# Kernel optimization log

Measured on AMD Instinct MI355X. Metric: run time of the kernel, lower is better.

Reference implementation:

```python
import jax, jax.numpy as jnp
import numpy as np

NEG_INF = -9e15  # matches torch's -9000000000000000.0 mask value
LEAKY_SLOPE = 0.2  # init alpha


def setup_inputs() -> dict:
    key = jax.random.key(0)
    k1, k2, k3, k4 = jax.random.split(key, 4)
    N, dim = 4096, 128
    hidden = jax.random.normal(k1, (N, dim), dtype=jnp.float32)
    adj = jax.random.randint(k2, (N, N), 0, 5)  # relation codes 0..4
    W = jax.random.normal(k3, (4, dim), dtype=jnp.float32) * (1.0 / np.sqrt(dim))
    b = jax.random.normal(k4, (4,), dtype=jnp.float32) * 0.01
    return {"hidden": hidden, "adj": adj, "W": W, "b": b}


def reference(hidden, adj, W, b):
    # e_k[i,j] = leakyrelu(sum_d h[i,d]*h[j,d]*W[k,d] + b[k])
    # equivalent to the torch repeat/view outer-product + four dim->1 Linears,
    # computed without materializing the [N,N,dim] intermediate.
    hw = hidden[None, :, :] * W[:, None, :]               # [4, N, dim]
    e = jnp.einsum('knd,md->knm', hw, hidden) + b[:, None, None]  # [4, N, N]
    e = jax.nn.leaky_relu(e, negative_slope=LEAKY_SLOPE)
    neg = jnp.asarray(NEG_INF, dtype=e.dtype)
    alpha = jnp.where(adj == 1, e[0], neg)
    alpha = jnp.where(adj == 2, e[1], alpha)
    alpha = jnp.where(adj == 3, e[2], alpha)
    alpha = jnp.where(adj == 4, e[3], alpha)
    alpha = jax.nn.softmax(alpha, axis=-1)                # [N, N]
    return alpha @ hidden                                  # [N, dim]
```

## Files before the change

kernel.cpp:

```cpp
#include <hip/hip_runtime.h>

#define NN 4096
#define DIM 128
#define TN 64
#define TM 128
#define NSPLIT 4
#define NTILES 8

typedef __attribute__((ext_vector_type(8))) short bf16x8;
typedef __attribute__((ext_vector_type(4))) float f32x4;

#define LSTRIDE 136
#define REGION  (128 * LSTRIDE)
#define TILE_USH (2 * REGION)
#define TILE_CHUNKS 68
#define PST 136

__device__ inline unsigned short f2bf(float x) {
    union { float f; unsigned u; } v; v.f = x;
    unsigned r = v.u + 0x7FFFu + ((v.u >> 16) & 1u);
    return (unsigned short)(r >> 16);
}

__device__ inline void dma16(const void* g, void* l) {
    __builtin_amdgcn_global_load_lds(
        (const __attribute__((address_space(1))) void*)g,
        (__attribute__((address_space(3))) void*)l,
        16, 0, 0);
}

__global__ __launch_bounds__(256) void prep_pack_kernel(
    const float* __restrict__ hidden,
    unsigned short* __restrict__ Hpack)
{
    __shared__ unsigned short T[16][LSTRIDE];
    const int tid = threadIdx.x;
    const int t0  = blockIdx.x >> 3;
    const int s   = blockIdx.x & 7;
    const int m0  = t0 * TM;
    unsigned short* rowdst = Hpack + (size_t)t0 * TILE_USH;
    unsigned short* coldst = rowdst + REGION;

    #pragma unroll
    for (int it = 0; it < 2; ++it) {
        int idx = tid + 256 * it;
        int row = idx >> 5;
        int c4  = (idx & 31) * 4;
        float4 v = *(const float4*)(hidden + (size_t)(m0 + 16 * s + row) * DIM + c4);
        ushort4 o;
        o.x = f2bf(v.x); o.y = f2bf(v.y); o.z = f2bf(v.z); o.w = f2bf(v.w);
        *(ushort4*)(rowdst + (16 * s + row) * LSTRIDE + c4) = o;
    }
    #pragma unroll
    for (int it = 0; it < 2; ++it) {
        int idx = tid + 256 * it;
        int m  = idx >> 2;
        int dc = (idx & 3) * 4;
        float4 v = *(const float4*)(hidden + (size_t)(m0 + m) * DIM + 16 * s + dc);
        T[dc + 0][m] = f2bf(v.x);
        T[dc + 1][m] = f2bf(v.y);
        T[dc + 2][m] = f2bf(v.z);
        T[dc + 3][m] = f2bf(v.w);
    }
    __syncthreads();
    {
        int d  = tid >> 4;
        int c8 = (tid & 15) * 8;
        uint4 v = *(const uint4*)(&T[d][c8]);
        *(uint4*)(coldst + (16 * s + d) * LSTRIDE + c8) = v;
    }
}

__global__ __launch_bounds__(512, 2) void gat_flash_kernel(
    const float* __restrict__ hidden,
    const unsigned short* __restrict__ Hpack,
    const int*   __restrict__ adj,
    const float* __restrict__ W,
    const float* __restrict__ bvec,
    float*       __restrict__ Opart,
    float*       __restrict__ lpart)
{
    __shared__ __align__(16) unsigned short HH[2][TILE_USH];
    __shared__ __align__(16) unsigned short Plc[TN * PST];
    __shared__ float redsum[8][16];

    const int tid  = threadIdx.x;
    const int w    = tid >> 6;
    const int lane = tid & 63;
    const int g    = lane >> 4;
    const int l15  = lane & 15;
    const int blk  = blockIdx.x;
    const int nbr  = blk >> 2;
    const int q4   = blk & 3;
    const int n0   = nbr * TN;
    const int gt0  = q4 * NTILES;
    const int rg   = w >> 1;
    const int msw  = w & 1;
    const int lofs = lane * 16;
    const float NEG = -9.0e15f;

    const float b0 = bvec[0], b1 = bvec[1], b2 = bvec[2], b3 = bvec[3];

    {
        const char* src = (const char*)(Hpack + (size_t)gt0 * TILE_USH);
        char* dst = (char*)&HH[0][0];
        #pragma unroll
        for (int it = 0; it < 9; ++it) {
            int chunk = it * 8 + w;
            if (chunk < TILE_CHUNKS)
                dma16(src + chunk * 1024 + lofs, dst + chunk * 1024);
        }
    }
    {
        #pragma unroll
        for (int it = 0; it < 4; ++it) {
            int idx = tid + 512 * it;
            int row = idx >> 3;
            int c16 = (idx & 7) * 16;
            int k = row >> 6, r = row & 63;
            const float* hrow = hidden + (size_t)(n0 + r) * DIM + c16;
            const float* wrow = W + k * DIM + c16;
            unsigned short* qdst = &HH[1][row * LSTRIDE + c16];
            #pragma unroll
            for (int c = 0; c < 4; ++c) {
                float4 hv = *(const float4*)(hrow + 4 * c);
                float4 wv = *(const float4*)(wrow + 4 * c);
                ushort4 o;
                o.x = f2bf(hv.x * wv.x); o.y = f2bf(hv.y * wv.y);
                o.z = f2bf(hv.z * wv.z); o.w = f2bf(hv.w * wv.w);
                *(ushort4*)(qdst + 4 * c) = o;
            }
        }
    }
    __syncthreads();

    bf16x8 Af[4][4];
    #pragma unroll
    for (int k = 0; k < 4; ++k)
        #pragma unroll
        for (int ks = 0; ks < 4; ++ks)
            Af[k][ks] = *(const bf16x8*)&HH[1][(k * 64 + rg * 16 + l15) * LSTRIDE + ks * 32 + 8 * g];
    __syncthreads();

    float lrow[4] = {0.f, 0.f, 0.f, 0.f};
    f32x4 Oacc[4];
    #pragma unroll
    for (int dt = 0; dt < 4; ++dt) Oacc[dt] = (f32x4){0.f, 0.f, 0.f, 0.f};

    const size_t arow = (size_t)(n0 + rg * 16 + 4 * g) * NN;
    int avc[16], avn[16];
    #pragma unroll
    for (int ch = 0; ch < 4; ++ch)
        #pragma unroll
        for (int t = 0; t < 4; ++t)
            avc[ch * 4 + t] = adj[arow + (size_t)t * NN + gt0 * TM + msw * 64 + ch * 16 + l15];

    for (int tile = 0; tile < NTILES; ++tile) {
        const int cur = tile & 1;
        const int nxt = cur ^ 1;

        if (tile + 1 < NTILES) {
            const char* src = (const char*)(Hpack + (size_t)(gt0 + tile + 1) * TILE_USH);
            char* dst = (char*)&HH[nxt][0];
            #pragma unroll
            for (int it = 0; it < 9; ++it) {
                int chunk = it * 8 + w;
                if (chunk < TILE_CHUNKS)
                    dma16(src + chunk * 1024 + lofs, dst + chunk * 1024);
            }
            #pragma unroll
            for (int ch = 0; ch < 4; ++ch)
                #pragma unroll
                for (int t = 0; t < 4; ++t)
                    avn[ch * 4 + t] = adj[arow + (size_t)t * NN + (gt0 + tile + 1) * TM + msw * 64 + ch * 16 + l15];
        }

        f32x4 S[4][4];
        #pragma unroll
        for (int k = 0; k < 4; ++k)
            #pragma unroll
            for (int ch = 0; ch < 4; ++ch)
                S[k][ch] = (f32x4){0.f, 0.f, 0.f, 0.f};
        #pragma unroll
        for (int ks = 0; ks < 4; ++ks) {
            #pragma unroll
            for (int ch = 0; ch < 4; ++ch) {
                bf16x8 B = *(const bf16x8*)&HH[cur][(msw * 64 + ch * 16 + l15) * LSTRIDE + ks * 32 + 8 * g];
                #pragma unroll
                for (int k = 0; k < 4; ++k)
                    S[k][ch] = __builtin_amdgcn_mfma_f32_16x16x32_bf16(Af[k][ks], B, S[k][ch], 0, 0, 0);
            }
        }

        #pragma unroll
        for (int ch = 0; ch < 4; ++ch) {
            #pragma unroll
            for (int t = 0; t < 4; ++t) {
                int a = avc[ch * 4 + t];
                float s = S[0][ch][t] + b0;
                s = (a == 2) ? S[1][ch][t] + b1 : s;
                s = (a == 3) ? S[2][ch][t] + b2 : s;
                s = (a == 4) ? S[3][ch][t] + b3 : s;
                float e = fmaxf(s, 0.2f * s);
                e = (a == 0) ? NEG : e;
                float p = __expf(e);
                lrow[t] += p;
                Plc[(rg * 16 + 4 * g + t) * PST + msw * 64 + ch * 16 + l15] = f2bf(p);
            }
        }

        asm volatile("s_waitcnt lgkmcnt(0)\n\ts_barrier" ::: "memory");

        #pragma unroll
        for (int c4 = 0; c4 < 4; ++c4) {
            bf16x8 Pa = *(const bf16x8*)&Plc[(rg * 16 + l15) * PST + c4 * 32 + 8 * g];
            #pragma unroll
            for (int dt = 0; dt < 4; ++dt) {
                bf16x8 Bv = *(const bf16x8*)&HH[cur][REGION + (msw * 64 + dt * 16 + l15) * LSTRIDE + c4 * 32 + 8 * g];
                Oacc[dt] = __builtin_amdgcn_mfma_f32_16x16x32_bf16(Pa, Bv, Oacc[dt], 0, 0, 0);
            }
        }

        #pragma unroll
        for (int i = 0; i < 16; ++i) avc[i] = avn[i];
        __syncthreads();
    }

    #pragma unroll
    for (int t = 0; t < 4; ++t) {
        float v = lrow[t];
        v += __shfl_xor(v, 1); v += __shfl_xor(v, 2);
        v += __shfl_xor(v, 4); v += __shfl_xor(v, 8);
        if (l15 == 0) redsum[w][4 * g + t] = v;
    }
    __syncthreads();
    if (tid < TN) {
        int rg2 = tid >> 4, rr = tid & 15;
        lpart[blk * TN + tid] = redsum[rg2 * 2 + 0][rr] + redsum[rg2 * 2 + 1][rr];
    }
    float* Ob = Opart + (size_t)blk * (TN * DIM);
    #pragma unroll
    for (int dt = 0; dt < 4; ++dt)
        #pragma unroll
        for (int t = 0; t < 4; ++t)
            Ob[(rg * 16 + 4 * g + t) * DIM + msw * 64 + dt * 16 + l15] = Oacc[dt][t];
}

__global__ __launch_bounds__(256) void combine_kernel(
    const float* __restrict__ Opart, const float* __restrict__ lpart,
    float* __restrict__ out)
{
    int idx = blockIdx.x * 256 + threadIdx.x;
    int r = idx >> 7, d = idx & 127;
    int nbr = r >> 6, rr = r & 63;
    float O = 0.f, l = 0.f;
    #pragma unroll
    for (int q = 0; q < NSPLIT; ++q) {
        O += Opart[(size_t)(nbr * NSPLIT + q) * (TN * DIM) + rr * 128 + d];
        l += lpart[(nbr * NSPLIT + q) * TN + rr];
    }
    out[idx] = O / l;
}

extern "C" void kernel_launch(void* const* d_in, const int* in_sizes, int n_in,
                              void* d_out, int out_size, void* d_ws, size_t ws_size,
                              hipStream_t stream) {
    const float* hidden = (const float*)d_in[0];
    const int*   adj    = (const int*)d_in[1];
    const float* W      = (const float*)d_in[2];
    const float* b      = (const float*)d_in[3];
    float* out = (float*)d_out;

    char* ws = (char*)d_ws;
    unsigned short* Hpack = (unsigned short*)ws;
    float* Opart = (float*)(ws + (4u << 20));
    float* lpart = (float*)(ws + (12u << 20));

    prep_pack_kernel<<<(NN / TM) * 8, 256, 0, stream>>>(hidden, Hpack);
    gat_flash_kernel<<<256, 512, 0, stream>>>(hidden, Hpack, adj, W, b, Opart, lpart);
    combine_kernel<<<NN * DIM / 256, 256, 0, stream>>>(Opart, lpart, out);
}
```

Baseline: 131.5 us.

## Double threads per block to 1024 and split tile columns across four warps

The flash-style GAT kernel now launches 1024 threads per block, so 16 waves each own 32 columns of a tile instead of 64. Per-wave score and output accumulators shrink, and the score MFMAs are interleaved per column chunk to cut register pressure. The aim is more latency hiding within each block, since there are only 256 blocks. The masked case now zeroes the probability after exp rather than feeding a huge negative into exp. The trade-off is that each wave reloads the same A fragments for less work, and the larger block may not fit two blocks per CU.

```diff
diff --git a/kernel.cpp b/kernel.cpp
--- a/kernel.cpp
+++ b/kernel.cpp
@@ -71,7 +71,7 @@
     }
 }
 
-__global__ __launch_bounds__(512, 2) void gat_flash_kernel(
+__global__ __launch_bounds__(1024) void gat_flash_kernel(
     const float* __restrict__ hidden,
     const unsigned short* __restrict__ Hpack,
     const int*   __restrict__ adj,
@@ -82,7 +82,7 @@
 {
     __shared__ __align__(16) unsigned short HH[2][TILE_USH];
     __shared__ __align__(16) unsigned short Plc[TN * PST];
-    __shared__ float redsum[8][16];
+    __shared__ float redsum[16][16];
 
     const int tid  = threadIdx.x;
     const int w    = tid >> 6;
@@ -94,10 +94,9 @@
     const int q4   = blk & 3;
     const int n0   = nbr * TN;
     const int gt0  = q4 * NTILES;
-    const int rg   = w >> 1;
-    const int msw  = w & 1;
+    const int rg   = w >> 2;
+    const int msw  = w & 3;
     const int lofs = lane * 16;
-    const float NEG = -9.0e15f;
 
     const float b0 = bvec[0], b1 = bvec[1], b2 = bvec[2], b3 = bvec[3];
 
@@ -105,16 +104,16 @@
         const char* src = (const char*)(Hpack + (size_t)gt0 * TILE_USH);
         char* dst = (char*)&HH[0][0];
         #pragma unroll
-        for (int it = 0; it < 9; ++it) {
-            int chunk = it * 8 + w;
+        for (int it = 0; it < 5; ++it) {
+            int chunk = it * 16 + w;
             if (chunk < TILE_CHUNKS)
                 dma16(src + chunk * 1024 + lofs, dst + chunk * 1024);
         }
     }
     {
         #pragma unroll
-        for (int it = 0; it < 4; ++it) {
-            int idx = tid + 512 * it;
+        for (int it = 0; it < 2; ++it) {
+            int idx = tid + 1024 * it;
             int row = idx >> 3;
             int c16 = (idx & 7) * 16;
             int k = row >> 6, r = row & 63;
@@ -143,17 +142,17 @@
     __syncthreads();
 
     float lrow[4] = {0.f, 0.f, 0.f, 0.f};
-    f32x4 Oacc[4];
-    #pragma unroll
-    for (int dt = 0; dt < 4; ++dt) Oacc[dt] = (f32x4){0.f, 0.f, 0.f, 0.f};
+    f32x4 Oacc[2];
+    #pragma unroll
+    for (int dt = 0; dt < 2; ++dt) Oacc[dt] = (f32x4){0.f, 0.f, 0.f, 0.f};
 
     const size_t arow = (size_t)(n0 + rg * 16 + 4 * g) * NN;
-    int avc[16], avn[16];
-    #pragma unroll
-    for (int ch = 0; ch < 4; ++ch)
+    int avc[8], avn[8];
+    #pragma unroll
+    for (int ch = 0; ch < 2; ++ch)
         #pragma unroll
         for (int t = 0; t < 4; ++t)
-            avc[ch * 4 + t] = adj[arow + (size_t)t * NN + gt0 * TM + msw * 64 + ch * 16 + l15];
+            avc[ch * 4 + t] = adj[arow + (size_t)t * NN + gt0 * TM + msw * 32 + ch * 16 + l15];
 
     for (int tile = 0; tile < NTILES; ++tile) {
         const int cur = tile & 1;
@@ -163,49 +162,42 @@
             const char* src = (const char*)(Hpack + (size_t)(gt0 + tile + 1) * TILE_USH);
             char* dst = (char*)&HH[nxt][0];
             #pragma unroll
-            for (int it = 0; it < 9; ++it) {
-                int chunk = it * 8 + w;
+            for (int it = 0; it < 5; ++it) {
+                int chunk = it * 16 + w;
                 if (chunk < TILE_CHUNKS)
                     dma16(src + chunk * 1024 + lofs, dst + chunk * 1024);
             }
             #pragma unroll
-            for (int ch = 0; ch < 4; ++ch)
+            for (int ch = 0; ch < 2; ++ch)
                 #pragma unroll
                 for (int t = 0; t < 4; ++t)
-                    avn[ch * 4 + t] = adj[arow + (size_t)t * NN + (gt0 + tile + 1) * TM + msw * 64 + ch * 16 + l15];
-        }
-
-        f32x4 S[4][4];
-        #pragma unroll
-        for (int k = 0; k < 4; ++k)
-            #pragma unroll
-            for (int ch = 0; ch < 4; ++ch)
-                S[k][ch] = (f32x4){0.f, 0.f, 0.f, 0.f};
-        #pragma unroll
-        for (int ks = 0; ks < 4; ++ks) {
-            #pragma unroll
-            for (int ch = 0; ch < 4; ++ch) {
-                bf16x8 B = *(const bf16x8*)&HH[cur][(msw * 64 + ch * 16 + l15) * LSTRIDE + ks * 32 + 8 * g];
+                    avn[ch * 4 + t] = adj[arow + (size_t)t * NN + (size_t)(gt0 + tile + 1) * TM + msw * 32 + ch * 16 + l15];
+        }
+
+        #pragma unroll
+        for (int ch = 0; ch < 2; ++ch) {
+            f32x4 S[4];
+            #pragma unroll
+            for (int k = 0; k < 4; ++k) S[k] = (f32x4){0.f, 0.f, 0.f, 0.f};
+            #pragma unroll
+            for (int ks = 0; ks < 4; ++ks) {
+                bf16x8 B = *(const bf16x8*)&HH[cur][(msw * 32 + ch * 16 + l15) * LSTRIDE + ks * 32 + 8 * g];
                 #pragma unroll
                 for (int k = 0; k < 4; ++k)
-                    S[k][ch] = __builtin_amdgcn_mfma_f32_16x16x32_bf16(Af[k][ks], B, S[k][ch], 0, 0, 0);
-            }
-        }
-
-        #pragma unroll
-        for (int ch = 0; ch < 4; ++ch) {
+                    S[k] = __builtin_amdgcn_mfma_f32_16x16x32_bf16(Af[k][ks], B, S[k], 0, 0, 0);
+            }
             #pragma unroll
             for (int t = 0; t < 4; ++t) {
                 int a = avc[ch * 4 + t];
-                float s = S[0][ch][t] + b0;
-                s = (a == 2) ? S[1][ch][t] + b1 : s;
-                s = (a == 3) ? S[2][ch][t] + b2 : s;
-                s = (a == 4) ? S[3][ch][t] + b3 : s;
+                float s = S[0][t] + b0;
+                s = (a == 2) ? S[1][t] + b1 : s;
+                s = (a == 3) ? S[2][t] + b2 : s;
+                s = (a == 4) ? S[3][t] + b3 : s;
                 float e = fmaxf(s, 0.2f * s);
-                e = (a == 0) ? NEG : e;
                 float p = __expf(e);
+                p = (a == 0) ? 0.f : p;
                 lrow[t] += p;
-                Plc[(rg * 16 + 4 * g + t) * PST + msw * 64 + ch * 16 + l15] = f2bf(p);
+                Plc[(rg * 16 + 4 * g + t) * PST + msw * 32 + ch * 16 + l15] = f2bf(p);
             }
         }
 
@@ -215,14 +207,14 @@
         for (int c4 = 0; c4 < 4; ++c4) {
             bf16x8 Pa = *(const bf16x8*)&Plc[(rg * 16 + l15) * PST + c4 * 32 + 8 * g];
             #pragma unroll
-            for (int dt = 0; dt < 4; ++dt) {
-                bf16x8 Bv = *(const bf16x8*)&HH[cur][REGION + (msw * 64 + dt * 16 + l15) * LSTRIDE + c4 * 32 + 8 * g];
+            for (int dt = 0; dt < 2; ++dt) {
+                bf16x8 Bv = *(const bf16x8*)&HH[cur][REGION + (msw * 32 + dt * 16 + l15) * LSTRIDE + c4 * 32 + 8 * g];
                 Oacc[dt] = __builtin_amdgcn_mfma_f32_16x16x32_bf16(Pa, Bv, Oacc[dt], 0, 0, 0);
             }
         }
 
         #pragma unroll
-        for (int i = 0; i < 16; ++i) avc[i] = avn[i];
+        for (int i = 0; i < 8; ++i) avc[i] = avn[i];
         __syncthreads();
     }
 
@@ -236,14 +228,15 @@
     __syncthreads();
     if (tid < TN) {
         int rg2 = tid >> 4, rr = tid & 15;
-        lpart[blk * TN + tid] = redsum[rg2 * 2 + 0][rr] + redsum[rg2 * 2 + 1][rr];
+        lpart[blk * TN + tid] = redsum[rg2 * 4 + 0][rr] + redsum[rg2 * 4 + 1][rr]
+                              + redsum[rg2 * 4 + 2][rr] + redsum[rg2 * 4 + 3][rr];
     }
     float* Ob = Opart + (size_t)blk * (TN * DIM);
     #pragma unroll
-    for (int dt = 0; dt < 4; ++dt)
+    for (int dt = 0; dt < 2; ++dt)
         #pragma unroll
         for (int t = 0; t < 4; ++t)
-            Ob[(rg * 16 + 4 * g + t) * DIM + msw * 64 + dt * 16 + l15] = Oacc[dt][t];
+            Ob[(rg * 16 + 4 * g + t) * DIM + msw * 32 + dt * 16 + l15] = Oacc[dt][t];
 }
 
 __global__ __launch_bounds__(256) void combine_kernel(
@@ -277,6 +270,6 @@
     float* lpart = (float*)(ws + (12u << 20));
 
     prep_pack_kernel<<<(NN / TM) * 8, 256, 0, stream>>>(hidden, Hpack);
-    gat_flash_kernel<<<256, 512, 0, stream>>>(hidden, Hpack, adj, W, b, Opart, lpart);
+    gat_flash_kernel<<<256, 1024, 0, stream>>>(hidden, Hpack, adj, W, b, Opart, lpart);
     combine_kernel<<<NN * DIM / 256, 256, 0, stream>>>(Opart, lpart, out);
 }
```

After: 254.1 us. +93.2%, slower.
